# Performance work log

Measured on AMD Instinct MI355X. Metric: run time of the kernel, lower is better.

The kernel has to match this reference:

```python
import jax, jax.numpy as jnp
import numpy as np

B, S, H = 64, 2048, 512


def setup_inputs() -> dict:
    key = jax.random.key(0)
    ks = jax.random.split(key, 11)
    sc = 1.0 / np.sqrt(H)
    return {
        "encoder_output": jax.random.normal(ks[0], (B, S, H), jnp.float32),
        "decoder_hidden": jax.random.normal(ks[1], (B, H), jnp.float32),
        "coverage": jax.random.uniform(ks[2], (B, S), jnp.float32),
        # params (torch Linear: y = x @ W.T + b); we store W already transposed as [in, out]
        "Wh": jax.random.normal(ks[3], (H, H), jnp.float32) * sc,
        "bh": jax.random.normal(ks[4], (H,), jnp.float32) * sc,
        "Ws": jax.random.normal(ks[5], (H, H), jnp.float32) * sc,
        "bs": jax.random.normal(ks[6], (H,), jnp.float32) * sc,
        "Wc": jax.random.normal(ks[7], (1, H), jnp.float32) * sc,  # Linear(1, H)
        "bc": jax.random.normal(ks[8], (H,), jnp.float32) * sc,
        "v_w": jax.random.normal(ks[9], (H,), jnp.float32) * sc,   # Linear(H, 1) weight
        "v_b": jax.random.normal(ks[10], (1,), jnp.float32) * sc,
    }


def reference(encoder_output, decoder_hidden, coverage, Wh, bh, Ws, bs, Wc, bc, v_w, v_b):
    # encoder_feature: [B,S,H]
    enc_f = jnp.einsum('bsh,hk->bsk', encoder_output, Wh) + bh
    # decoder_feature: [B,1,H]
    dec_f = (decoder_hidden @ Ws + bs)[:, None, :]
    # coverage_feature: [B,S,H] = cov[...,None] @ Wc(1,H) + bc
    cov_f = coverage[:, :, None] * Wc[0] + bc
    feat = jnp.tanh(enc_f + dec_f + cov_f)          # [B,S,H]
    e_t = jnp.einsum('bsh,h->bs', feat, v_w) + v_b[0]  # [B,S]
    a_t = jax.nn.softmax(e_t, axis=-1)
    sum_coverage = coverage + a_t
    return a_t, sum_coverage
```

## Files before the change

kernel.cpp:

```cpp
#include <hip/hip_runtime.h>
#include <math.h>


#define B_ 64
#define S_ 2048
#define H_ 512
#define M_ (B_ * S_)

#define BM 64
#define BN 256
#define BK 32
#define ASTRIDE 56

typedef __attribute__((ext_vector_type(4))) float f32x4;
typedef __attribute__((ext_vector_type(8))) short s16x8;
typedef __attribute__((ext_vector_type(4))) short s16x4;

typedef __attribute__((address_space(1))) void gvoid;
typedef __attribute__((address_space(3))) void lvoid;

__device__ __forceinline__ short f2bf(float f) {
    unsigned u = __float_as_uint(f);
    u += 0x7fffu + ((u >> 16) & 1u);
    return (short)(u >> 16);
}

__device__ __forceinline__ float fast_tanh(float x) {
    return 1.0f - 2.0f / (__expf(2.0f * x) + 1.0f);
}

__global__ __launch_bounds__(256) void transpose_cast(
    const float* __restrict__ Wh, short* __restrict__ Bt) {
    __shared__ float tile[32][33];
    const int n0 = blockIdx.x * 32, k0 = blockIdx.y * 32;
    const int tx = threadIdx.x & 31, ty = threadIdx.x >> 5;
#pragma unroll
    for (int r = 0; r < 32; r += 8)
        tile[ty + r][tx] = Wh[(size_t)(k0 + ty + r) * H_ + n0 + tx];
    __syncthreads();
#pragma unroll
    for (int r = 0; r < 32; r += 8)
        Bt[(size_t)(n0 + ty + r) * H_ + k0 + tx] = f2bf(tile[tx][ty + r]);
}

__global__ __launch_bounds__(512) void dec_kernel(
    const float* __restrict__ dh, const float* __restrict__ Ws,
    const float* __restrict__ bs, const float* __restrict__ bh,
    const float* __restrict__ bc, float* __restrict__ D) {
    const int b = blockIdx.x;
    const int h = threadIdx.x;
    __shared__ float sdh[H_];
    sdh[h] = dh[b * H_ + h];
    __syncthreads();
    float acc = bs[h] + bh[h] + bc[h];
#pragma unroll 8
    for (int k = 0; k < H_; ++k)
        acc = fmaf(sdh[k], Ws[k * H_ + h], acc);
    D[b * H_ + h] = acc;
}

__global__ __launch_bounds__(256, 3) void gemm_fused(
    const float* __restrict__ A,
    const short* __restrict__ Bt,
    const float* __restrict__ cover,
    const float* __restrict__ Wc,
    const float* __restrict__ vw,
    const float* __restrict__ D,
    float* __restrict__ e_ws) {
    __shared__ short As[BM * ASTRIDE];
    __shared__ __align__(16) short Bs[BN * BK];
    __shared__ float sWc[BN], sVw[BN], sD[BN], sCov[BM];
    __shared__ float part[4][BM];

    const int tid = threadIdx.x;
    const int w = tid >> 6;
    const int l = tid & 63;
    const int row0 = blockIdx.x * BM;
    const int n0 = blockIdx.y * BN;
    const int b = row0 >> 11;

    sWc[tid] = Wc[n0 + tid];
    sVw[tid] = vw[n0 + tid];
    sD[tid] = D[b * H_ + n0 + tid];
    if (tid < BM) sCov[tid] = cover[row0 + tid];

    const int am = tid >> 2;
    const int ak = (tid & 3) * 8;
    const float* aptr = A + (size_t)(row0 + am) * H_ + ak;
    short* adst = &As[am * ASTRIDE + ak];

    const int bkq = ((l & 3) - (l >> 3)) & 3;
    const int bn_off = w * 64 + (l >> 2);
    const short* bptr = Bt + (size_t)(n0 + bn_off) * H_ + bkq * 8;

    const int q = l >> 4;
    const int ml = l & 15;

    f32x4 acc[4][4];
#pragma unroll
    for (int i = 0; i < 4; ++i)
#pragma unroll
        for (int j = 0; j < 4; ++j) acc[i][j] = (f32x4)0.0f;

    float4 av0 = *(const float4*)(aptr);
    float4 av1 = *(const float4*)(aptr + 4);
    aptr += BK;

    for (int kk = 0; kk < H_; kk += BK) {
        s16x4 pk0, pk1;
        pk0.x = f2bf(av0.x); pk0.y = f2bf(av0.y);
        pk0.z = f2bf(av0.z); pk0.w = f2bf(av0.w);
        pk1.x = f2bf(av1.x); pk1.y = f2bf(av1.y);
        pk1.z = f2bf(av1.z); pk1.w = f2bf(av1.w);
        *(s16x4*)(adst) = pk0;
        *(s16x4*)(adst + 4) = pk1;

#pragma unroll
        for (int c = 0; c < 4; ++c) {
            __builtin_amdgcn_global_load_lds(
                (gvoid*)(bptr + (size_t)c * 16 * H_),
                (lvoid*)(Bs + (w * 4 + c) * 512),
                16, 0, 0);
        }
        bptr += BK;

        if (kk + BK < H_) {
            av0 = *(const float4*)(aptr);
            av1 = *(const float4*)(aptr + 4);
            aptr += BK;
        }
        __syncthreads();

        s16x8 afr[4], bfr[4];
#pragma unroll
        for (int mi = 0; mi < 4; ++mi)
            afr[mi] = *(const s16x8*)&As[(mi * 16 + ml) * ASTRIDE + q * 8];
#pragma unroll
        for (int ni = 0; ni < 4; ++ni) {
            const int n = w * 64 + ni * 16 + ml;
            bfr[ni] = *(const s16x8*)&Bs[n * BK + (((q + (n >> 1)) & 3) << 3)];
        }
#pragma unroll
        for (int mi = 0; mi < 4; ++mi)
#pragma unroll
            for (int ni = 0; ni < 4; ++ni)
                acc[mi][ni] = __builtin_amdgcn_mfma_f32_16x16x32_bf16(
                    afr[mi], bfr[ni], acc[mi][ni], 0, 0, 0);
        __syncthreads();
    }

#pragma unroll
    for (int mi = 0; mi < 4; ++mi) {
        const int rbase = mi * 16 + q * 4;
        const float cv0 = sCov[rbase + 0];
        const float cv1 = sCov[rbase + 1];
        const float cv2 = sCov[rbase + 2];
        const float cv3 = sCov[rbase + 3];
        float p0 = 0.f, p1 = 0.f, p2 = 0.f, p3 = 0.f;
#pragma unroll
        for (int ni = 0; ni < 4; ++ni) {
            const int n = w * 64 + ni * 16 + ml;
            const float wcv = sWc[n], ddv = sD[n], vvv = sVw[n];
            p0 += vvv * fast_tanh(acc[mi][ni].x + fmaf(cv0, wcv, ddv));
            p1 += vvv * fast_tanh(acc[mi][ni].y + fmaf(cv1, wcv, ddv));
            p2 += vvv * fast_tanh(acc[mi][ni].z + fmaf(cv2, wcv, ddv));
            p3 += vvv * fast_tanh(acc[mi][ni].w + fmaf(cv3, wcv, ddv));
        }
#pragma unroll
        for (int s = 1; s < 16; s <<= 1) {
            p0 += __shfl_xor(p0, s, 64);
            p1 += __shfl_xor(p1, s, 64);
            p2 += __shfl_xor(p2, s, 64);
            p3 += __shfl_xor(p3, s, 64);
        }
        if (ml == 0) {
            part[w][rbase + 0] = p0;
            part[w][rbase + 1] = p1;
            part[w][rbase + 2] = p2;
            part[w][rbase + 3] = p3;
        }
    }
    __syncthreads();
    if (tid < BM) {
        float e = part[0][tid] + part[1][tid] + part[2][tid] + part[3][tid];
        e_ws[(size_t)blockIdx.y * M_ + row0 + tid] = e;
    }
}

__global__ __launch_bounds__(256) void softmax_kernel(
    const float* __restrict__ e_ws, const float* __restrict__ cover,
    const float* __restrict__ vb, float* __restrict__ out) {
    const int b = blockIdx.x;
    const int tid = threadIdx.x;
    const float vbv = vb[0];

    float e[8];
    float mx = -1e30f;
#pragma unroll
    for (int r = 0; r < 8; ++r) {
        const int idx = b * S_ + r * 256 + tid;
        e[r] = e_ws[idx] + e_ws[M_ + idx] + vbv;
        mx = fmaxf(mx, e[r]);
    }
#pragma unroll
    for (int off = 32; off >= 1; off >>= 1) mx = fmaxf(mx, __shfl_xor(mx, off, 64));

    __shared__ float sm[4], ss[4], sbc[2];
    const int wid = tid >> 6, lane = tid & 63;
    if (lane == 0) sm[wid] = mx;
    __syncthreads();
    if (tid == 0) sbc[0] = fmaxf(fmaxf(sm[0], sm[1]), fmaxf(sm[2], sm[3]));
    __syncthreads();
    mx = sbc[0];

    float ex[8];
    float sum = 0.0f;
#pragma unroll
    for (int r = 0; r < 8; ++r) {
        ex[r] = __expf(e[r] - mx);
        sum += ex[r];
    }
#pragma unroll
    for (int off = 32; off >= 1; off >>= 1) sum += __shfl_xor(sum, off, 64);
    if (lane == 0) ss[wid] = sum;
    __syncthreads();
    if (tid == 0) sbc[1] = ss[0] + ss[1] + ss[2] + ss[3];
    __syncthreads();
    const float inv = 1.0f / sbc[1];

#pragma unroll
    for (int r = 0; r < 8; ++r) {
        const int s = r * 256 + tid;
        const float a = ex[r] * inv;
        out[b * S_ + s] = a;
        out[M_ + b * S_ + s] = cover[b * S_ + s] + a;
    }
}

extern "C" void kernel_launch(void* const* d_in, const int* in_sizes, int n_in,
                              void* d_out, int out_size, void* d_ws, size_t ws_size,
                              hipStream_t stream) {
    const float* enc = (const float*)d_in[0];
    const float* dh  = (const float*)d_in[1];
    const float* cov = (const float*)d_in[2];
    const float* Wh  = (const float*)d_in[3];
    const float* bh  = (const float*)d_in[4];
    const float* Ws  = (const float*)d_in[5];
    const float* bs  = (const float*)d_in[6];
    const float* Wc  = (const float*)d_in[7];
    const float* bc  = (const float*)d_in[8];
    const float* vw  = (const float*)d_in[9];
    const float* vb  = (const float*)d_in[10];
    float* out = (float*)d_out;

    float* e_ws = (float*)d_ws;
    float* Dws  = e_ws + 2 * M_;
    short* Whbt = (short*)(Dws + B_ * H_);

    transpose_cast<<<dim3(H_ / 32, H_ / 32), 256, 0, stream>>>(Wh, Whbt);
    dec_kernel<<<B_, 512, 0, stream>>>(dh, Ws, bs, bh, bc, Dws);
    dim3 g2(M_ / BM, H_ / BN);
    gemm_fused<<<g2, 256, 0, stream>>>(enc, Whbt, cov, Wc, vw, Dws, e_ws);
    softmax_kernel<<<B_, 256, 0, stream>>>(e_ws, cov, vb, out);
}
```

Before: 511.1 us.

## Restructure fused GEMM: A fragments from registers, half-K B tiles in LDS, N split by four

The fused GEMM is rewritten so that each warp loads its A rows straight from global memory into MFMA fragments in registers, skipping LDS staging for A. B is staged in LDS as a 128xK/2 swizzled tile loaded in two halves. The N dimension is split into four phases with 512-thread blocks of 256 rows, and partial e values are written to four workspace slices that softmax now sums. The A tile is therefore re-read from global memory four times instead of twice, and A-operand reads are uncoalesced per-lane row loads, in exchange for fewer barriers and larger B reuse.

```diff
diff --git a/kernel.cpp b/kernel.cpp
--- a/kernel.cpp
+++ b/kernel.cpp
@@ -7,22 +7,25 @@
 #define H_ 512
 #define M_ (B_ * S_)
 
-#define BM 64
-#define BN 256
-#define BK 32
-#define ASTRIDE 56
+#define BN 128
+#define PHASES 4
+#define KH 256
+#define RPB 256
 
 typedef __attribute__((ext_vector_type(4))) float f32x4;
 typedef __attribute__((ext_vector_type(8))) short s16x8;
-typedef __attribute__((ext_vector_type(4))) short s16x4;
-
-typedef __attribute__((address_space(1))) void gvoid;
-typedef __attribute__((address_space(3))) void lvoid;
 
 __device__ __forceinline__ short f2bf(float f) {
     unsigned u = __float_as_uint(f);
     u += 0x7fffu + ((u >> 16) & 1u);
     return (short)(u >> 16);
+}
+
+__device__ __forceinline__ s16x8 cvt8(float4 a, float4 b) {
+    s16x8 r;
+    r[0] = f2bf(a.x); r[1] = f2bf(a.y); r[2] = f2bf(a.z); r[3] = f2bf(a.w);
+    r[4] = f2bf(b.x); r[5] = f2bf(b.y); r[6] = f2bf(b.z); r[7] = f2bf(b.w);
+    return r;
 }
 
 __device__ __forceinline__ float fast_tanh(float x) {
@@ -59,7 +62,7 @@
     D[b * H_ + h] = acc;
 }
 
-__global__ __launch_bounds__(256, 3) void gemm_fused(
+__global__ __launch_bounds__(512, 4) void gemm_fused(
     const float* __restrict__ A,
     const short* __restrict__ Bt,
     const float* __restrict__ cover,
@@ -67,104 +70,102 @@
     const float* __restrict__ vw,
     const float* __restrict__ D,
     float* __restrict__ e_ws) {
-    __shared__ short As[BM * ASTRIDE];
-    __shared__ __align__(16) short Bs[BN * BK];
-    __shared__ float sWc[BN], sVw[BN], sD[BN], sCov[BM];
-    __shared__ float part[4][BM];
+    __shared__ __align__(16) short Bs[BN * KH];
 
     const int tid = threadIdx.x;
     const int w = tid >> 6;
     const int l = tid & 63;
-    const int row0 = blockIdx.x * BM;
-    const int n0 = blockIdx.y * BN;
-    const int b = row0 >> 11;
-
-    sWc[tid] = Wc[n0 + tid];
-    sVw[tid] = vw[n0 + tid];
-    sD[tid] = D[b * H_ + n0 + tid];
-    if (tid < BM) sCov[tid] = cover[row0 + tid];
-
-    const int am = tid >> 2;
-    const int ak = (tid & 3) * 8;
-    const float* aptr = A + (size_t)(row0 + am) * H_ + ak;
-    short* adst = &As[am * ASTRIDE + ak];
-
-    const int bkq = ((l & 3) - (l >> 3)) & 3;
-    const int bn_off = w * 64 + (l >> 2);
-    const short* bptr = Bt + (size_t)(n0 + bn_off) * H_ + bkq * 8;
-
     const int q = l >> 4;
     const int ml = l & 15;
 
-    f32x4 acc[4][4];
-#pragma unroll
-    for (int i = 0; i < 4; ++i)
-#pragma unroll
-        for (int j = 0; j < 4; ++j) acc[i][j] = (f32x4)0.0f;
-
-    float4 av0 = *(const float4*)(aptr);
-    float4 av1 = *(const float4*)(aptr + 4);
-    aptr += BK;
-
-    for (int kk = 0; kk < H_; kk += BK) {
-        s16x4 pk0, pk1;
-        pk0.x = f2bf(av0.x); pk0.y = f2bf(av0.y);
-        pk0.z = f2bf(av0.z); pk0.w = f2bf(av0.w);
-        pk1.x = f2bf(av1.x); pk1.y = f2bf(av1.y);
-        pk1.z = f2bf(av1.z); pk1.w = f2bf(av1.w);
-        *(s16x4*)(adst) = pk0;
-        *(s16x4*)(adst + 4) = pk1;
-
-#pragma unroll
-        for (int c = 0; c < 4; ++c) {
-            __builtin_amdgcn_global_load_lds(
-                (gvoid*)(bptr + (size_t)c * 16 * H_),
-                (lvoid*)(Bs + (w * 4 + c) * 512),
-                16, 0, 0);
-        }
-        bptr += BK;
-
-        if (kk + BK < H_) {
-            av0 = *(const float4*)(aptr);
-            av1 = *(const float4*)(aptr + 4);
-            aptr += BK;
+    const int phase = blockIdx.x;
+    const int n0 = phase * BN;
+    const int row_blk = blockIdx.y * RPB;
+    const int b = row_blk >> 11;
+    const int r0 = row_blk + w * 32;
+
+    f32x4 acc[2][8];
+#pragma unroll
+    for (int t = 0; t < 2; ++t)
+#pragma unroll
+        for (int u = 0; u < 8; ++u) acc[t][u] = (f32x4)0.0f;
+
+    const float* ap0 = A + (size_t)(r0 + ml) * H_ + q * 8;
+    const float* ap1 = ap0 + (size_t)16 * H_;
+    float4 pa0 = *(const float4*)ap0;
+    float4 pa1 = *(const float4*)(ap0 + 4);
+    float4 pa2 = *(const float4*)ap1;
+    float4 pa3 = *(const float4*)(ap1 + 4);
+    ap0 += 32; ap1 += 32;
+
+    const int sn = tid >> 2;
+    const int scb = (tid & 3) * 8;
+    const short* sg = Bt + (size_t)(n0 + sn) * H_ + scb * 8;
+    short* sd = Bs + sn * KH;
+
+    for (int half = 0; half < 2; ++half) {
+        if (half) __syncthreads();
+#pragma unroll
+        for (int j = 0; j < 8; ++j) {
+            const int c = scb + j;
+            const int cs = c ^ (sn & 7);
+            *(s16x8*)(sd + cs * 8) = *(const s16x8*)(sg + j * 8 + half * KH);
         }
         __syncthreads();
 
-        s16x8 afr[4], bfr[4];
-#pragma unroll
-        for (int mi = 0; mi < 4; ++mi)
-            afr[mi] = *(const s16x8*)&As[(mi * 16 + ml) * ASTRIDE + q * 8];
-#pragma unroll
-        for (int ni = 0; ni < 4; ++ni) {
-            const int n = w * 64 + ni * 16 + ml;
-            bfr[ni] = *(const s16x8*)&Bs[n * BK + (((q + (n >> 1)) & 3) << 3)];
-        }
-#pragma unroll
-        for (int mi = 0; mi < 4; ++mi)
-#pragma unroll
-            for (int ni = 0; ni < 4; ++ni)
-                acc[mi][ni] = __builtin_amdgcn_mfma_f32_16x16x32_bf16(
-                    afr[mi], bfr[ni], acc[mi][ni], 0, 0, 0);
-        __syncthreads();
-    }
-
-#pragma unroll
-    for (int mi = 0; mi < 4; ++mi) {
-        const int rbase = mi * 16 + q * 4;
-        const float cv0 = sCov[rbase + 0];
-        const float cv1 = sCov[rbase + 1];
-        const float cv2 = sCov[rbase + 2];
-        const float cv3 = sCov[rbase + 3];
+#pragma unroll
+        for (int ks = 0; ks < 8; ++ks) {
+            const s16x8 a0 = cvt8(pa0, pa1);
+            const s16x8 a1 = cvt8(pa2, pa3);
+            if (!(half == 1 && ks == 7)) {
+                pa0 = *(const float4*)ap0;
+                pa1 = *(const float4*)(ap0 + 4);
+                pa2 = *(const float4*)ap1;
+                pa3 = *(const float4*)(ap1 + 4);
+                ap0 += 32; ap1 += 32;
+            }
+            const int cbase = ks * 4 + q;
+#pragma unroll
+            for (int uh = 0; uh < 2; ++uh) {
+                s16x8 bfr[4];
+#pragma unroll
+                for (int v = 0; v < 4; ++v) {
+                    const int n = (uh * 4 + v) * 16 + ml;
+                    bfr[v] = *(const s16x8*)&Bs[n * KH + (cbase ^ (n & 7)) * 8];
+                }
+#pragma unroll
+                for (int v = 0; v < 4; ++v) {
+                    acc[0][uh * 4 + v] = __builtin_amdgcn_mfma_f32_16x16x32_bf16(
+                        a0, bfr[v], acc[0][uh * 4 + v], 0, 0, 0);
+                    acc[1][uh * 4 + v] = __builtin_amdgcn_mfma_f32_16x16x32_bf16(
+                        a1, bfr[v], acc[1][uh * 4 + v], 0, 0, 0);
+                }
+            }
+        }
+    }
+
+    float wc[8], vv[8], dd[8];
+#pragma unroll
+    for (int u = 0; u < 8; ++u) {
+        const int n = n0 + u * 16 + ml;
+        wc[u] = Wc[n];
+        vv[u] = vw[n];
+        dd[u] = D[b * H_ + n];
+    }
+#pragma unroll
+    for (int t = 0; t < 2; ++t) {
+        const int rb = r0 + t * 16 + q * 4;
         float p0 = 0.f, p1 = 0.f, p2 = 0.f, p3 = 0.f;
-#pragma unroll
-        for (int ni = 0; ni < 4; ++ni) {
-            const int n = w * 64 + ni * 16 + ml;
-            const float wcv = sWc[n], ddv = sD[n], vvv = sVw[n];
-            p0 += vvv * fast_tanh(acc[mi][ni].x + fmaf(cv0, wcv, ddv));
-            p1 += vvv * fast_tanh(acc[mi][ni].y + fmaf(cv1, wcv, ddv));
-            p2 += vvv * fast_tanh(acc[mi][ni].z + fmaf(cv2, wcv, ddv));
-            p3 += vvv * fast_tanh(acc[mi][ni].w + fmaf(cv3, wcv, ddv));
+        const float cv0 = cover[rb + 0];
+        const float cv1 = cover[rb + 1];
+        const float cv2 = cover[rb + 2];
+        const float cv3 = cover[rb + 3];
+#pragma unroll
+        for (int u = 0; u < 8; ++u) {
+            p0 += vv[u] * fast_tanh(acc[t][u].x + fmaf(cv0, wc[u], dd[u]));
+            p1 += vv[u] * fast_tanh(acc[t][u].y + fmaf(cv1, wc[u], dd[u]));
+            p2 += vv[u] * fast_tanh(acc[t][u].z + fmaf(cv2, wc[u], dd[u]));
+            p3 += vv[u] * fast_tanh(acc[t][u].w + fmaf(cv3, wc[u], dd[u]));
         }
 #pragma unroll
         for (int s = 1; s < 16; s <<= 1) {
@@ -174,16 +175,9 @@
             p3 += __shfl_xor(p3, s, 64);
         }
         if (ml == 0) {
-            part[w][rbase + 0] = p0;
-            part[w][rbase + 1] = p1;
-            part[w][rbase + 2] = p2;
-            part[w][rbase + 3] = p3;
-        }
-    }
-    __syncthreads();
-    if (tid < BM) {
-        float e = part[0][tid] + part[1][tid] + part[2][tid] + part[3][tid];
-        e_ws[(size_t)blockIdx.y * M_ + row0 + tid] = e;
+            float* dst = e_ws + (size_t)phase * M_ + rb;
+            dst[0] = p0; dst[1] = p1; dst[2] = p2; dst[3] = p3;
+        }
     }
 }
 
@@ -199,7 +193,8 @@
 #pragma unroll
     for (int r = 0; r < 8; ++r) {
         const int idx = b * S_ + r * 256 + tid;
-        e[r] = e_ws[idx] + e_ws[M_ + idx] + vbv;
+        e[r] = e_ws[idx] + e_ws[M_ + idx] + e_ws[2 * M_ + idx] +
+               e_ws[3 * M_ + idx] + vbv;
         mx = fmaxf(mx, e[r]);
     }
 #pragma unroll
@@ -254,12 +249,12 @@
     float* out = (float*)d_out;
 
     float* e_ws = (float*)d_ws;
-    float* Dws  = e_ws + 2 * M_;
+    float* Dws  = e_ws + PHASES * M_;
     short* Whbt = (short*)(Dws + B_ * H_);
 
     transpose_cast<<<dim3(H_ / 32, H_ / 32), 256, 0, stream>>>(Wh, Whbt);
     dec_kernel<<<B_, 512, 0, stream>>>(dh, Ws, bs, bh, bc, Dws);
-    dim3 g2(M_ / BM, H_ / BN);
-    gemm_fused<<<g2, 256, 0, stream>>>(enc, Whbt, cov, Wc, vw, Dws, e_ws);
+    dim3 g2(PHASES, M_ / RPB);
+    gemm_fused<<<g2, 512, 0, stream>>>(enc, Whbt, cov, Wc, vw, Dws, e_ws);
     softmax_kernel<<<B_, 256, 0, stream>>>(e_ws, cov, vb, out);
 }
```

Result: slower. 542.4 us (+6.1%).
